# Optimization experiments

Hardware: AMD Instinct MI355X
Metric: run time of the kernel (lower is better)

## Reference

```python
import jax, jax.numpy as jnp
import numpy as np

H = 8          # num heads
LN_EPS = 1e-5  # torch LayerNorm default

_SHAPES = {
    'src': (1024, 8, 256), 'pos': (1024, 8, 256), 'query_embed': (80, 8, 256), 'cam_mask': (8, 80, 1024),
    'enc_qkv_w': (2, 768, 256), 'enc_qkv_b': (2, 768), 'enc_out_w': (2, 256, 256), 'enc_out_b': (2, 256),
    'enc_ln1_g': (2, 256), 'enc_ln1_b': (2, 256),
    'enc_ff1_w': (2, 2048, 256), 'enc_ff1_b': (2, 2048), 'enc_ff2_w': (2, 256, 2048), 'enc_ff2_b': (2, 256),
    'enc_ln2_g': (2, 256), 'enc_ln2_b': (2, 256),
    'dec_sa_qkv_w': (2, 768, 256), 'dec_sa_qkv_b': (2, 768), 'dec_sa_out_w': (2, 256, 256), 'dec_sa_out_b': (2, 256),
    'dec_ln1_g': (2, 256), 'dec_ln1_b': (2, 256),
    'dec_ca_qkv_w': (2, 768, 256), 'dec_ca_qkv_b': (2, 768), 'dec_ca_out_w': (2, 256, 256), 'dec_ca_out_b': (2, 256),
    'dec_ln2_g': (2, 256), 'dec_ln2_b': (2, 256),
    'dec_ff1_w': (2, 2048, 256), 'dec_ff1_b': (2, 2048), 'dec_ff2_w': (2, 256, 2048), 'dec_ff2_b': (2, 256),
    'dec_ln3_g': (2, 256), 'dec_ln3_b': (2, 256),
    'dec_norm_g': (256,), 'dec_norm_b': (256,),
}


def setup_inputs() -> dict:
    key = jax.random.key(0)
    out = {}
    for i, (name, sh) in enumerate(_SHAPES.items()):
        k = jax.random.fold_in(key, i)
        if name.endswith('_g'):
            out[name] = jnp.ones(sh, jnp.float32)
        elif name.endswith('ln1_b') or name.endswith('ln2_b') or name.endswith('ln3_b') or name == 'dec_norm_b':
            out[name] = jnp.zeros(sh, jnp.float32)
        else:
            scale = 1.0 if name in ('src', 'pos', 'query_embed', 'cam_mask') else 0.02
            out[name] = jax.random.normal(k, sh, dtype=jnp.float32) * scale
    return out


def layer_norm(x, g, b):
    mu = jnp.mean(x, axis=-1, keepdims=True)
    var = jnp.mean(jnp.square(x - mu), axis=-1, keepdims=True)
    return (x - mu) * jax.lax.rsqrt(var + LN_EPS) * g + b


def mha(q_in, k_in, v_in, qkv_w, qkv_b, out_w, out_b, bias=None):
    # q_in: [L,B,D], k_in/v_in: [S,B,D]; torch layout: projections are x @ W.T + b
    L, B, D = q_in.shape
    S = k_in.shape[0]
    hd = D // H
    wq, wk, wv = qkv_w[:D], qkv_w[D:2 * D], qkv_w[2 * D:]
    bq, bk, bv = qkv_b[:D], qkv_b[D:2 * D], qkv_b[2 * D:]
    q = (q_in @ wq.T + bq).reshape(L, B, H, hd).transpose(1, 2, 0, 3)  # [B,H,L,hd]
    k = (k_in @ wk.T + bk).reshape(S, B, H, hd).transpose(1, 2, 0, 3)  # [B,H,S,hd]
    v = (v_in @ wv.T + bv).reshape(S, B, H, hd).transpose(1, 2, 0, 3)
    logits = jnp.einsum('bhld,bhsd->bhls', q, k) * (1.0 / np.sqrt(hd))
    if bias is not None:
        logits = logits + bias[:, None, :, :]  # CAM bias broadcast over heads
    attn = jax.nn.softmax(logits, axis=-1)
    o = jnp.einsum('bhls,bhsd->bhld', attn, v).transpose(2, 0, 1, 3).reshape(L, B, D)
    return o @ out_w.T + out_b


def reference(src, pos, query_embed, cam_mask,
              enc_qkv_w, enc_qkv_b, enc_out_w, enc_out_b, enc_ln1_g, enc_ln1_b,
              enc_ff1_w, enc_ff1_b, enc_ff2_w, enc_ff2_b, enc_ln2_g, enc_ln2_b,
              dec_sa_qkv_w, dec_sa_qkv_b, dec_sa_out_w, dec_sa_out_b, dec_ln1_g, dec_ln1_b,
              dec_ca_qkv_w, dec_ca_qkv_b, dec_ca_out_w, dec_ca_out_b, dec_ln2_g, dec_ln2_b,
              dec_ff1_w, dec_ff1_b, dec_ff2_w, dec_ff2_b, dec_ln3_g, dec_ln3_b,
              dec_norm_g, dec_norm_b):
    n_enc = enc_qkv_w.shape[0]
    n_dec = dec_sa_qkv_w.shape[0]
    # --- encoder (post-norm DETR style, pos added to q,k) ---
    mem = src
    for i in range(n_enc):
        qk = mem + pos
        a = mha(qk, qk, mem, enc_qkv_w[i], enc_qkv_b[i], enc_out_w[i], enc_out_b[i])
        mem = layer_norm(mem + a, enc_ln1_g[i], enc_ln1_b[i])
        f = jax.nn.relu(mem @ enc_ff1_w[i].T + enc_ff1_b[i]) @ enc_ff2_w[i].T + enc_ff2_b[i]
        mem = layer_norm(mem + f, enc_ln2_g[i], enc_ln2_b[i])
    # --- decoder: tgt starts at zeros (Q2L), query_embed is query_pos ---
    tgt = jnp.zeros_like(query_embed)
    for i in range(n_dec):
        qk = tgt + query_embed
        sa = mha(qk, qk, tgt, dec_sa_qkv_w[i], dec_sa_qkv_b[i], dec_sa_out_w[i], dec_sa_out_b[i])
        tgt = layer_norm(tgt + sa, dec_ln1_g[i], dec_ln1_b[i])
        ca = mha(tgt + query_embed, mem + pos, mem,
                 dec_ca_qkv_w[i], dec_ca_qkv_b[i], dec_ca_out_w[i], dec_ca_out_b[i],
                 bias=cam_mask)  # MA: CAM-derived additive attention bias [B,L,S]
        tgt = layer_norm(tgt + ca, dec_ln2_g[i], dec_ln2_b[i])
        f = jax.nn.relu(tgt @ dec_ff1_w[i].T + dec_ff1_b[i]) @ dec_ff2_w[i].T + dec_ff2_b[i]
        tgt = layer_norm(tgt + f, dec_ln3_g[i], dec_ln3_b[i])
    out = layer_norm(tgt, dec_norm_g, dec_norm_b)
    return out[None]  # [1, L, B, D] as in TransformerDecoder's output.unsqueeze(0)
```

## Files before the change

### kernel.cpp

```cpp
#include <hip/hip_runtime.h>
#include <hip/hip_bf16.h>
#include <cstdint>
#include <cstddef>

typedef __hip_bfloat16 bf16;
typedef float f4 __attribute__((ext_vector_type(4)));
typedef float f32x4 __attribute__((ext_vector_type(4)));
typedef short s8v __attribute__((ext_vector_type(8)));
typedef unsigned short u16x4 __attribute__((ext_vector_type(4)));

#define LN_EPS 1e-5f
#define LOG2E 1.4426950408889634f

__device__ __forceinline__ void async_cp16(const void* g, void* lds) {
  __builtin_amdgcn_global_load_lds(
      (const __attribute__((address_space(1))) unsigned int*)g,
      (__attribute__((address_space(3))) unsigned int*)lds, 16, 0, 0);
}

__device__ __forceinline__ uint32_t pkbf(float lo, float hi) {
  bf16 a = __float2bfloat16(lo), c = __float2bfloat16(hi);
  return (uint32_t)*(unsigned short*)&a | ((uint32_t)*(unsigned short*)&c << 16);
}

#define NCAST 11
struct CastArgs {
  const float* in[NCAST];
  bf16* out[NCAST];
  int end4[NCAST];
  int nseg;
};

__global__ __launch_bounds__(256) void cast_multi(CastArgs a, int total4) {
  int i = blockIdx.x * 256 + threadIdx.x;
  if (i >= total4) return;
  int s = 0;
  while (i >= a.end4[s]) ++s;
  int j = i - (s ? a.end4[s - 1] : 0);
  f4 v = ((const f4*)a.in[s])[j];
  u16x4 o;
#pragma unroll
  for (int c = 0; c < 4; ++c) {
    bf16 h = __float2bfloat16(v[c]);
    o[c] = *reinterpret_cast<unsigned short*>(&h);
  }
  ((u16x4*)a.out[s])[j] = o;
}

__global__ __launch_bounds__(256) void scale_f32_kernel(const float* __restrict__ in,
                                                        float* __restrict__ out,
                                                        float s, int n4) {
  int i = blockIdx.x * 256 + threadIdx.x;
  if (i < n4) {
    f4 v = ((const f4*)in)[i];
    ((f4*)out)[i] = v * s;
  }
}

__global__ __launch_bounds__(256) void add_bf16_kernel(const float* __restrict__ a,
                                                       const float* __restrict__ b,
                                                       bf16* __restrict__ out, int n4) {
  int i = blockIdx.x * 256 + threadIdx.x;
  if (i < n4) {
    f4 x = ((const f4*)a)[i];
    f4 y = ((const f4*)b)[i];
    u16x4 o;
#pragma unroll
    for (int j = 0; j < 4; ++j) {
      bf16 h = __float2bfloat16(x[j] + y[j]);
      o[j] = *reinterpret_cast<unsigned short*>(&h);
    }
    ((u16x4*)out)[i] = o;
  }
}

template <int TB, int MODE, int SPLITK>
__global__ __launch_bounds__(256, 2) void mfma_gemm(
    const bf16* __restrict__ A, const bf16* __restrict__ W,
    const float* __restrict__ bias, float* __restrict__ C,
    bf16* __restrict__ Cb, int M, int N, int K, int HL, float qscale) {
  constexpr int WM = TB / 2, WN = TB / 2;
  constexpr int MR = WM / 16, NR = WN / 16;
  constexpr int NCH = TB / 32;
  __shared__ __attribute__((aligned(16))) unsigned short As[TB][64];
  __shared__ __attribute__((aligned(16))) unsigned short Ws[TB][64];
  const int tid = threadIdx.x;
  const int lane = tid & 63, wave = tid >> 6;
  const int wr = wave >> 1, wc = wave & 1;
  const int bm = blockIdx.x * TB, bn = blockIdx.y * TB;
  const int fr = lane & 15, fo = lane >> 4;
  const int srowi = lane >> 3;
  const int slot = lane & 7;
  const int gcol = (slot ^ srowi) * 8;

  const int kchunk = K / SPLITK;
  const int kbeg = (SPLITK > 1) ? blockIdx.z * kchunk : 0;

  f32x4 acc[MR][NR] = {};

  for (int k0 = kbeg; k0 < kbeg + kchunk; k0 += 64) {
    __syncthreads();
#pragma unroll
    for (int c = 0; c < NCH; ++c) {
      int rbase = wave * (TB / 4) + c * 8;
      int row = rbase + srowi;
      async_cp16(A + (size_t)(bm + row) * K + k0 + gcol, &As[rbase][0]);
      async_cp16(W + (size_t)(bn + row) * K + k0 + gcol, &Ws[rbase][0]);
    }
    __syncthreads();
#pragma unroll
    for (int ks = 0; ks < 2; ++ks) {
      s8v a[MR], b[NR];
#pragma unroll
      for (int mi = 0; mi < MR; ++mi) {
        int row = wr * WM + mi * 16 + fr;
        a[mi] = *(const s8v*)((const char*)&As[0][0] + row * 128 +
                              ((ks * 64 + fo * 16) ^ ((row & 7) << 4)));
      }
#pragma unroll
      for (int ni = 0; ni < NR; ++ni) {
        int row = wc * WN + ni * 16 + fr;
        b[ni] = *(const s8v*)((const char*)&Ws[0][0] + row * 128 +
                              ((ks * 64 + fo * 16) ^ ((row & 7) << 4)));
      }
#pragma unroll
      for (int mi = 0; mi < MR; ++mi)
#pragma unroll
        for (int ni = 0; ni < NR; ++ni)
          acc[mi][ni] = __builtin_amdgcn_mfma_f32_16x16x32_bf16(
              a[mi], b[ni], acc[mi][ni], 0, 0, 0);
    }
  }

  const int r0 = (lane >> 4) * 4;
  float* Cz = (MODE == 4) ? C + (size_t)blockIdx.z * M * N : C;
#pragma unroll
  for (int mi = 0; mi < MR; ++mi) {
#pragma unroll
    for (int ni = 0; ni < NR; ++ni) {
      int col = bn + wc * WN + ni * 16 + fr;
      float bv = (MODE == 4) ? 0.f : bias[col];
#pragma unroll
      for (int r = 0; r < 4; ++r) {
        int row = bm + wr * WM + mi * 16 + r0 + r;
        float t = acc[mi][ni][r] + bv;
        if (MODE == 2) t = fmaxf(t, 0.f);
        if (MODE == 0) {
          C[(size_t)row * N + col] = t;
        } else if (MODE == 4) {
          Cz[(size_t)row * N + col] = t;
        } else if (MODE == 3) {
          int l = row >> 3, bb = row & 7;
          int sec = col >> 8, hh = (col >> 5) & 7, d = col & 31;
          if (sec == 0) t *= qscale;
          Cb[(size_t)sec * ((size_t)64 * HL * 32) +
             ((size_t)(bb * 8 + hh) * HL + l) * 32 + d] = __float2bfloat16(t);
        } else if (MODE == 5) {
          int l = row >> 3, bb = row & 7;
          int hh = (col >> 5) & 7, d = col & 31;
          Cb[((size_t)(bb * 8 + hh) * 32 + d) * HL + l] = __float2bfloat16(t);
        } else {
          Cb[(size_t)row * N + col] = __float2bfloat16(t);
        }
      }
    }
  }
}

template <int HAS_BIAS, int PARTIAL>
__global__ __launch_bounds__(256, 4) void attn_mfma(
    const bf16* __restrict__ Qh, const bf16* __restrict__ Kh,
    const bf16* __restrict__ VhT, const float* __restrict__ bias,
    bf16* __restrict__ O, float* __restrict__ PO, float* __restrict__ PM,
    float* __restrict__ PL, int L, int S, int SC) {
  __shared__ __attribute__((aligned(16))) uint32_t Ps2[4][16][36];
  const int tid = threadIdx.x;
  const int lane = tid & 63, wave = tid >> 6;
  const int fr = lane & 15, fo = lane >> 4;
  const int bh = blockIdx.x;
  const int b = bh >> 3, h = bh & 7;
  const int q0 = blockIdx.y * 64 + wave * 16;
  const int q = q0 + fr;

  const int cz = PARTIAL ? blockIdx.z : 0;
  const int sb = PARTIAL ? cz * SC : 0;
  const int se = PARTIAL ? min(S, sb + SC) : S;

  s8v qf = {};
  if (q < L) qf = *(const s8v*)(Qh + ((size_t)bh * L + q) * 32 + fo * 8);

  const float* brow = nullptr;
  if (HAS_BIAS) brow = bias + ((size_t)b * L + (q < L ? q : L - 1)) * S;

  float m = -1e30f, lsum = 0.f;
  f32x4 oacc[2] = {};

  s8v kf[4];
#pragma unroll
  for (int kb = 0; kb < 4; ++kb)
    kf[kb] = *(const s8v*)(Kh + ((size_t)bh * S + sb + kb * 16 + fr) * 32 + fo * 8);

  for (int s0 = sb; s0 < se; s0 += 64) {
    const bool more = (s0 + 64 < se);
    s8v kn[4];
    if (more) {
#pragma unroll
      for (int kb = 0; kb < 4; ++kb)
        kn[kb] = *(const s8v*)(Kh + ((size_t)bh * S + s0 + 64 + kb * 16 + fr) * 32 + fo * 8);
    }
    s8v vf[2][2];
#pragma unroll
    for (int dh = 0; dh < 2; ++dh)
#pragma unroll
      for (int ks = 0; ks < 2; ++ks)
        vf[dh][ks] = *(const s8v*)(VhT + ((size_t)bh * 32 + dh * 16 + fr) * S +
                                   s0 + ks * 32 + fo * 8);
    f4 bias4[4];
    if (HAS_BIAS) {
#pragma unroll
      for (int kb = 0; kb < 4; ++kb)
        bias4[kb] = *(const f4*)(brow + s0 + kb * 16 + 4 * fo);
    }

    f32x4 sa[4];
#pragma unroll
    for (int kb = 0; kb < 4; ++kb) {
      f32x4 z = {};
      sa[kb] = __builtin_amdgcn_mfma_f32_16x16x32_bf16(kf[kb], qf, z, 0, 0, 0);
    }

    float lg[16];
#pragma unroll
    for (int kb = 0; kb < 4; ++kb)
#pragma unroll
      for (int r = 0; r < 4; ++r)
        lg[kb * 4 + r] = HAS_BIAS ? sa[kb][r] + bias4[kb][r] : sa[kb][r];

    if (s0 + 64 > se) {
#pragma unroll
      for (int kb = 0; kb < 4; ++kb)
#pragma unroll
        for (int r = 0; r < 4; ++r)
          if (s0 + kb * 16 + 4 * fo + r >= se) lg[kb * 4 + r] = -1e30f;
    }

    float tm = lg[0];
#pragma unroll
    for (int i = 1; i < 16; ++i) tm = fmaxf(tm, lg[i]);
    tm = fmaxf(tm, __shfl_xor(tm, 16));
    tm = fmaxf(tm, __shfl_xor(tm, 32));

    if (__any(tm > m + 8.f)) {
      float nm = fmaxf(m, tm);
      float rs = exp2f(m - nm);
      m = nm;
      lsum *= rs;
#pragma unroll
      for (int r = 0; r < 4; ++r) { oacc[0][r] *= rs; oacc[1][r] *= rs; }
    }

    float pr[16];
    float ps = 0.f;
#pragma unroll
    for (int i = 0; i < 16; ++i) {
      pr[i] = exp2f(lg[i] - m);
      ps += pr[i];
    }
    lsum += ps;

#pragma unroll
    for (int kb = 0; kb < 4; ++kb) {
      uint32_t w0 = pkbf(pr[kb * 4 + 0], pr[kb * 4 + 1]);
      uint32_t w1 = pkbf(pr[kb * 4 + 2], pr[kb * 4 + 3]);
      uint64_t w = (uint64_t)w0 | ((uint64_t)w1 << 32);
      *(uint64_t*)&Ps2[wave][fr][kb * 8 + 2 * fo] = w;
    }

    s8v pf[2];
#pragma unroll
    for (int ks = 0; ks < 2; ++ks)
      pf[ks] = *(const s8v*)&Ps2[wave][fr][ks * 16 + 4 * fo];

#pragma unroll
    for (int dh = 0; dh < 2; ++dh)
#pragma unroll
      for (int ks = 0; ks < 2; ++ks)
        oacc[dh] = __builtin_amdgcn_mfma_f32_16x16x32_bf16(
            vf[dh][ks], pf[ks], oacc[dh], 0, 0, 0);

    if (more) {
#pragma unroll
      for (int kb = 0; kb < 4; ++kb) kf[kb] = kn[kb];
    }
  }

  lsum += __shfl_xor(lsum, 16);
  lsum += __shfl_xor(lsum, 32);

  if (q < L) {
    if (PARTIAL) {
      size_t pi = ((size_t)cz * 64 + bh) * L + q;
      float* po = PO + pi * 32;
#pragma unroll
      for (int dh = 0; dh < 2; ++dh) {
        f4 t;
#pragma unroll
        for (int r = 0; r < 4; ++r) t[r] = oacc[dh][r];
        *(f4*)(po + dh * 16 + 4 * fo) = t;
      }
      if (fo == 0) { PM[pi] = m; PL[pi] = lsum; }
    } else {
      float inv = 1.f / lsum;
      bf16* op = O + ((size_t)q * 8 + b) * 256 + h * 32;
#pragma unroll
      for (int dh = 0; dh < 2; ++dh) {
        uint32_t w0 = pkbf(oacc[dh][0] * inv, oacc[dh][1] * inv);
        uint32_t w1 = pkbf(oacc[dh][2] * inv, oacc[dh][3] * inv);
        *(uint32_t*)(op + dh * 16 + 4 * fo) = w0;
        *(uint32_t*)(op + dh * 16 + 4 * fo + 2) = w1;
      }
    }
  }
}

__global__ __launch_bounds__(256) void attn_combine(
    const float* __restrict__ PO, const float* __restrict__ PM,
    const float* __restrict__ PL, bf16* __restrict__ O, int L, int NC) {
  int gid = blockIdx.x * 256 + threadIdx.x;
  if (gid >= 64 * L * 32) return;
  int d = gid & 31;
  int rem = gid >> 5;
  int q = rem % L, bh = rem / L;
  int b = bh >> 3, h = bh & 7;
  float M = -1e30f;
  for (int c = 0; c < NC; ++c) M = fmaxf(M, PM[((size_t)c * 64 + bh) * L + q]);
  float lsum = 0.f, o = 0.f;
  for (int c = 0; c < NC; ++c) {
    size_t pi = ((size_t)c * 64 + bh) * L + q;
    float w = exp2f(PM[pi] - M);
    lsum += PL[pi] * w;
    o += PO[pi * 32 + d] * w;
  }
  O[((size_t)q * 8 + b) * 256 + h * 32 + d] = __float2bfloat16(o / lsum);
}

__global__ __launch_bounds__(256) void ln_kernel(
    const float* __restrict__ x, const float* __restrict__ res,
    const float* __restrict__ parts, int nparts, int pstride,
    const float* __restrict__ gbias,
    const float* __restrict__ g, const float* __restrict__ b,
    float* __restrict__ out, bf16* __restrict__ outb) {
  const int row = blockIdx.x, tid = threadIdx.x;
  size_t idx = (size_t)row * 256 + tid;
  float v = x[idx];
  if (res) v += res[idx];
  if (parts) {
    for (int z = 0; z < nparts; ++z) v += parts[(size_t)z * pstride + idx];
  }
  if (gbias) v += gbias[tid];
  float s = v, s2 = v * v;
#pragma unroll
  for (int off = 32; off >= 1; off >>= 1) {
    s += __shfl_down(s, off);
    s2 += __shfl_down(s2, off);
  }
  __shared__ float red[8];
  int wv = tid >> 6;
  if ((tid & 63) == 0) { red[wv] = s; red[4 + wv] = s2; }
  __syncthreads();
  if (tid == 0) {
    float ts = red[0] + red[1] + red[2] + red[3];
    float ts2 = red[4] + red[5] + red[6] + red[7];
    float mu = ts * (1.f / 256.f);
    float var = ts2 * (1.f / 256.f) - mu * mu;
    red[0] = mu;
    red[1] = rsqrtf(var + LN_EPS);
  }
  __syncthreads();
  float y = (v - red[0]) * red[1] * g[tid] + b[tid];
  if (out) out[idx] = y;
  if (outb) outb[idx] = __float2bfloat16(y);
}

extern "C" void kernel_launch(void* const* d_in, const int* in_sizes, int n_in,
                              void* d_out, int out_size, void* d_ws, size_t ws_size,
                              hipStream_t stream) {
  const float* src         = (const float*)d_in[0];
  const float* pos         = (const float*)d_in[1];
  const float* query_embed = (const float*)d_in[2];
  const float* cam_mask    = (const float*)d_in[3];
  const float* enc_qkv_w   = (const float*)d_in[4];
  const float* enc_qkv_b   = (const float*)d_in[5];
  const float* enc_out_w   = (const float*)d_in[6];
  const float* enc_out_b   = (const float*)d_in[7];
  const float* enc_ln1_g   = (const float*)d_in[8];
  const float* enc_ln1_b   = (const float*)d_in[9];
  const float* enc_ff1_w   = (const float*)d_in[10];
  const float* enc_ff1_b   = (const float*)d_in[11];
  const float* enc_ff2_w   = (const float*)d_in[12];
  const float* enc_ff2_b   = (const float*)d_in[13];
  const float* enc_ln2_g   = (const float*)d_in[14];
  const float* enc_ln2_b   = (const float*)d_in[15];
  const float* dec_sa_qkv_w= (const float*)d_in[16];
  const float* dec_sa_qkv_b= (const float*)d_in[17];
  const float* dec_sa_out_w= (const float*)d_in[18];
  const float* dec_sa_out_b= (const float*)d_in[19];
  const float* dec_ln1_g   = (const float*)d_in[20];
  const float* dec_ln1_b   = (const float*)d_in[21];
  const float* dec_ca_qkv_w= (const float*)d_in[22];
  const float* dec_ca_qkv_b= (const float*)d_in[23];
  const float* dec_ca_out_w= (const float*)d_in[24];
  const float* dec_ca_out_b= (const float*)d_in[25];
  const float* dec_ln2_g   = (const float*)d_in[26];
  const float* dec_ln2_b   = (const float*)d_in[27];
  const float* dec_ff1_w   = (const float*)d_in[28];
  const float* dec_ff1_b   = (const float*)d_in[29];
  const float* dec_ff2_w   = (const float*)d_in[30];
  const float* dec_ff2_b   = (const float*)d_in[31];
  const float* dec_ln3_g   = (const float*)d_in[32];
  const float* dec_ln3_b   = (const float*)d_in[33];
  const float* dec_norm_g  = (const float*)d_in[34];
  const float* dec_norm_b  = (const float*)d_in[35];

  size_t off = 0;
  char* base = (char*)d_ws;
  auto af = [&](size_t n) { float* p = (float*)(base + off); off += n * 4; return p; };
  auto ab = [&](size_t n) { bf16*  p = (bf16*)(base + off);  off += n * 2; return p; };

  float* mem  = af(2097152);
  float* r1   = af(2097152);
  float* PO   = af(8388608);
  float* pm   = af(262144);
  float* pl   = af(262144);
  float* cmlog= af(655360);
  float* tgt  = af(163840);
  float* tpr  = af(163840);
  bf16* memb  = ab(2097152);
  bf16* qkb   = ab(2097152);
  bf16* aob   = ab(2097152);
  bf16* ffb   = ab(16777216);
  bf16* bufQ  = ab(4194304);
  bf16* bufK  = ab(2097152);
  bf16* bufV  = ab(2097152);
  bf16* tgtb  = ab(163840);
  bf16* tqkb  = ab(163840);
  bf16* taob  = ab(163840);
  bf16* tffb  = ab(1310720);
  bf16* w_enc_qkv = ab(393216);
  bf16* w_enc_out = ab(131072);
  bf16* w_enc_ff1 = ab(1048576);
  bf16* w_enc_ff2 = ab(1048576);
  bf16* w_sa_qkv  = ab(393216);
  bf16* w_sa_out  = ab(131072);
  bf16* w_ca_qkv  = ab(393216);
  bf16* w_ca_out  = ab(131072);
  bf16* w_dec_ff1 = ab(1048576);
  bf16* w_dec_ff2 = ab(1048576);

  const float qscale = 0.17677669529663687f * LOG2E;

  {
    CastArgs ca;
    const float* ins[NCAST] = {enc_qkv_w, enc_out_w, enc_ff1_w, enc_ff2_w,
                               dec_sa_qkv_w, dec_sa_out_w, dec_ca_qkv_w,
                               dec_ca_out_w, dec_ff1_w, dec_ff2_w, src};
    bf16* outs[NCAST] = {w_enc_qkv, w_enc_out, w_enc_ff1, w_enc_ff2,
                         w_sa_qkv, w_sa_out, w_ca_qkv,
                         w_ca_out, w_dec_ff1, w_dec_ff2, memb};
    int n4s[NCAST] = {98304, 32768, 262144, 262144, 98304, 32768, 98304,
                      32768, 262144, 262144, 524288};
    int acc = 0;
    for (int s = 0; s < NCAST; ++s) {
      ca.in[s] = ins[s]; ca.out[s] = outs[s];
      acc += n4s[s]; ca.end4[s] = acc;
    }
    ca.nseg = NCAST;
    cast_multi<<<(acc + 255) / 256, 256, 0, stream>>>(ca, acc);
  }
  scale_f32_kernel<<<640, 256, 0, stream>>>(cam_mask, cmlog, LOG2E, 163840);
  hipMemcpyAsync(mem, src, (size_t)2097152 * 4, hipMemcpyDeviceToDevice, stream);

  auto g64_f = [&](const bf16* A, const bf16* W, const float* bias, float* C,
                   int M, int N, int K) {
    mfma_gemm<64, 0, 1><<<dim3(M / 64, N / 64), 256, 0, stream>>>(
        A, W, bias, C, nullptr, M, N, K, 0, 1.f);
  };
  auto g64_head = [&](const bf16* A, const bf16* W, const float* bias, bf16* Cb,
                      int M, int N, int K, int HL, float qs) {
    mfma_gemm<64, 3, 1><<<dim3(M / 64, N / 64), 256, 0, stream>>>(
        A, W, bias, nullptr, Cb, M, N, K, HL, qs);
  };
  auto g64_headT = [&](const bf16* A, const bf16* W, const float* bias, bf16* Cb,
                       int M, int N, int K, int HL) {
    mfma_gemm<64, 5, 1><<<dim3(M / 64, N / 64), 256, 0, stream>>>(
        A, W, bias, nullptr, Cb, M, N, K, HL, 1.f);
  };
  auto g64_relu = [&](const bf16* A, const bf16* W, const float* bias, bf16* Cb,
                      int M, int N, int K) {
    mfma_gemm<64, 2, 1><<<dim3(M / 64, N / 64), 256, 0, stream>>>(
        A, W, bias, nullptr, Cb, M, N, K, 0, 1.f);
  };
  auto g128_relu = [&](const bf16* A, const bf16* W, const float* bias, bf16* Cb,
                       int M, int N, int K) {
    mfma_gemm<128, 2, 1><<<dim3(M / 128, N / 128), 256, 0, stream>>>(
        A, W, bias, nullptr, Cb, M, N, K, 0, 1.f);
  };

  for (int i = 0; i < 2; ++i) {
    const bf16* wq = w_enc_qkv + (size_t)i * 196608;
    const float* qkvb = enc_qkv_b + (size_t)i * 768;
    add_bf16_kernel<<<2048, 256, 0, stream>>>(mem, pos, qkb, 524288);
    g64_head(qkb, wq, qkvb, bufQ, 8192, 512, 256, 1024, qscale);
    g64_headT(memb, wq + 131072, qkvb + 512, bufV, 8192, 256, 256, 1024);
    attn_mfma<0, 0><<<dim3(64, 16), 256, 0, stream>>>(
        bufQ, bufQ + 2097152, bufV, nullptr, aob, nullptr, nullptr, nullptr,
        1024, 1024, 0);
    g64_f(aob, w_enc_out + (size_t)i * 65536, enc_out_b + i * 256, r1,
          8192, 256, 256);
    ln_kernel<<<8192, 256, 0, stream>>>(mem, r1, nullptr, 0, 0, nullptr,
                                        enc_ln1_g + i * 256, enc_ln1_b + i * 256,
                                        mem, memb);
    g128_relu(memb, w_enc_ff1 + (size_t)i * 524288, enc_ff1_b + i * 2048, ffb,
              8192, 2048, 256);
    mfma_gemm<128, 4, 4><<<dim3(64, 2, 4), 256, 0, stream>>>(
        ffb, w_enc_ff2 + (size_t)i * 524288, nullptr, PO, nullptr,
        8192, 256, 2048, 0, 1.f);
    ln_kernel<<<8192, 256, 0, stream>>>(mem, nullptr, PO, 4, 2097152,
                                        enc_ff2_b + i * 256,
                                        enc_ln2_g + i * 256, enc_ln2_b + i * 256,
                                        mem, memb);
  }

  hipMemsetAsync(tgt, 0, (size_t)163840 * 4, stream);
  hipMemsetAsync(tgtb, 0, (size_t)163840 * 2, stream);
  add_bf16_kernel<<<2048, 256, 0, stream>>>(mem, pos, qkb, 524288);

  for (int i = 0; i < 2; ++i) {
    const bf16* wsa = w_sa_qkv + (size_t)i * 196608;
    const float* sab = dec_sa_qkv_b + (size_t)i * 768;
    const bf16* wca = w_ca_qkv + (size_t)i * 196608;
    const float* cab = dec_ca_qkv_b + (size_t)i * 768;

    add_bf16_kernel<<<160, 256, 0, stream>>>(tgt, query_embed, tqkb, 40960);
    g64_head(tqkb, wsa, sab, bufQ, 640, 512, 256, 80, qscale);
    g64_headT(tgtb, wsa + 131072, sab + 512, bufV, 640, 256, 256, 80);
    attn_mfma<0, 0><<<dim3(64, 2), 256, 0, stream>>>(
        bufQ, bufQ + 163840, bufV, nullptr, taob, nullptr, nullptr, nullptr,
        80, 80, 0);
    g64_f(taob, w_sa_out + (size_t)i * 65536, dec_sa_out_b + i * 256, tpr,
          640, 256, 256);
    ln_kernel<<<640, 256, 0, stream>>>(tgt, tpr, nullptr, 0, 0, nullptr,
                                       dec_ln1_g + i * 256, dec_ln1_b + i * 256,
                                       tgt, tgtb);
    add_bf16_kernel<<<160, 256, 0, stream>>>(tgt, query_embed, tqkb, 40960);
    g64_head(tqkb, wca, cab, bufQ, 640, 256, 256, 80, qscale);
    g64_head(qkb, wca + 65536, cab + 256, bufK, 8192, 256, 256, 1024, 1.f);
    g64_headT(memb, wca + 131072, cab + 512, bufV, 8192, 256, 256, 1024);
    attn_mfma<1, 1><<<dim3(64, 2, 8), 256, 0, stream>>>(
        bufQ, bufK, bufV, cmlog, nullptr, PO, pm, pl, 80, 1024, 128);
    attn_combine<<<640, 256, 0, stream>>>(PO, pm, pl, taob, 80, 8);
    g64_f(taob, w_ca_out + (size_t)i * 65536, dec_ca_out_b + i * 256, tpr,
          640, 256, 256);
    ln_kernel<<<640, 256, 0, stream>>>(tgt, tpr, nullptr, 0, 0, nullptr,
                                       dec_ln2_g + i * 256, dec_ln2_b + i * 256,
                                       tgt, tgtb);
    g64_relu(tgtb, w_dec_ff1 + (size_t)i * 524288, dec_ff1_b + i * 2048, tffb,
             640, 2048, 256);
    mfma_gemm<64, 4, 4><<<dim3(10, 4, 4), 256, 0, stream>>>(
        tffb, w_dec_ff2 + (size_t)i * 524288, nullptr, PO, nullptr,
        640, 256, 2048, 0, 1.f);
    ln_kernel<<<640, 256, 0, stream>>>(tgt, nullptr, PO, 4, 163840,
                                       dec_ff2_b + i * 256,
                                       dec_ln3_g + i * 256, dec_ln3_b + i * 256,
                                       tgt, tgtb);
  }

  ln_kernel<<<640, 256, 0, stream>>>(tgt, nullptr, nullptr, 0, 0, nullptr,
                                     dec_norm_g, dec_norm_b,
                                     (float*)d_out, nullptr);
}
```

Measured before the change: 462.0 us.

## Batch decoder cross-attn K/V projections for both layers; split-K encoder attention

The memory-side K and V projections for cross-attention depend only on the final encoder memory, so both decoder layers' K/V weights are packed together and projected in one wide GEMM pair before the decoder loop. This replaces four smaller per-layer GEMMs with two larger ones. It needs reshuffled weight casts, a concatenated bias buffer and a section-aware transposed-V epilogue. Encoder self-attention is also switched to a two-way split over keys with a combine kernel, adding parallelism at the cost of extra partial-output traffic.

```diff
diff --git a/kernel.cpp b/kernel.cpp
--- a/kernel.cpp
+++ b/kernel.cpp
@@ -23,7 +23,7 @@
   return (uint32_t)*(unsigned short*)&a | ((uint32_t)*(unsigned short*)&c << 16);
 }
 
-#define NCAST 11
+#define NCAST 16
 struct CastArgs {
   const float* in[NCAST];
   bf16* out[NCAST];
@@ -157,8 +157,9 @@
              ((size_t)(bb * 8 + hh) * HL + l) * 32 + d] = __float2bfloat16(t);
         } else if (MODE == 5) {
           int l = row >> 3, bb = row & 7;
-          int hh = (col >> 5) & 7, d = col & 31;
-          Cb[((size_t)(bb * 8 + hh) * 32 + d) * HL + l] = __float2bfloat16(t);
+          int sec = col >> 8, hh = (col >> 5) & 7, d = col & 31;
+          Cb[(size_t)sec * ((size_t)64 * 32 * HL) +
+             ((size_t)(bb * 8 + hh) * 32 + d) * HL + l] = __float2bfloat16(t);
         } else {
           Cb[(size_t)row * N + col] = __float2bfloat16(t);
         }
@@ -433,6 +434,7 @@
   float* pm   = af(262144);
   float* pl   = af(262144);
   float* cmlog= af(655360);
+  float* pb   = af(1024);
   float* tgt  = af(163840);
   float* tpr  = af(163840);
   bf16* memb  = ab(2097152);
@@ -440,8 +442,9 @@
   bf16* aob   = ab(2097152);
   bf16* ffb   = ab(16777216);
   bf16* bufQ  = ab(4194304);
-  bf16* bufK  = ab(2097152);
-  bf16* bufV  = ab(2097152);
+  bf16* bufK  = ab(4194304);
+  bf16* bufV  = ab(4194304);
+  bf16* bufVsa= ab(163840);
   bf16* tgtb  = ab(163840);
   bf16* tqkb  = ab(163840);
   bf16* taob  = ab(163840);
@@ -452,7 +455,8 @@
   bf16* w_enc_ff2 = ab(1048576);
   bf16* w_sa_qkv  = ab(393216);
   bf16* w_sa_out  = ab(131072);
-  bf16* w_ca_qkv  = ab(393216);
+  bf16* w_ca_q    = ab(131072);
+  bf16* w_ca_kv   = ab(262144);
   bf16* w_ca_out  = ab(131072);
   bf16* w_dec_ff1 = ab(1048576);
   bf16* w_dec_ff2 = ab(1048576);
@@ -461,13 +465,28 @@
 
   {
     CastArgs ca;
-    const float* ins[NCAST] = {enc_qkv_w, enc_out_w, enc_ff1_w, enc_ff2_w,
-                               dec_sa_qkv_w, dec_sa_out_w, dec_ca_qkv_w,
-                               dec_ca_out_w, dec_ff1_w, dec_ff2_w, src};
-    bf16* outs[NCAST] = {w_enc_qkv, w_enc_out, w_enc_ff1, w_enc_ff2,
-                         w_sa_qkv, w_sa_out, w_ca_qkv,
-                         w_ca_out, w_dec_ff1, w_dec_ff2, memb};
-    int n4s[NCAST] = {98304, 32768, 262144, 262144, 98304, 32768, 98304,
+    const float* ins[NCAST] = {
+        enc_qkv_w, enc_out_w, enc_ff1_w, enc_ff2_w,
+        dec_sa_qkv_w, dec_sa_out_w,
+        dec_ca_qkv_w,
+        dec_ca_qkv_w + 65536,
+        dec_ca_qkv_w + 131072,
+        dec_ca_qkv_w + 196608,
+        dec_ca_qkv_w + 262144,
+        dec_ca_qkv_w + 327680,
+        dec_ca_out_w, dec_ff1_w, dec_ff2_w, src};
+    bf16* outs[NCAST] = {
+        w_enc_qkv, w_enc_out, w_enc_ff1, w_enc_ff2,
+        w_sa_qkv, w_sa_out,
+        w_ca_q,
+        w_ca_kv,
+        w_ca_kv + 131072,
+        w_ca_q + 65536,
+        w_ca_kv + 65536,
+        w_ca_kv + 196608,
+        w_ca_out, w_dec_ff1, w_dec_ff2, memb};
+    int n4s[NCAST] = {98304, 32768, 262144, 262144, 98304, 32768,
+                      16384, 16384, 16384, 16384, 16384, 16384,
                       32768, 262144, 262144, 524288};
     int acc = 0;
     for (int s = 0; s < NCAST; ++s) {
@@ -479,6 +498,10 @@
   }
   scale_f32_kernel<<<640, 256, 0, stream>>>(cam_mask, cmlog, LOG2E, 163840);
   hipMemcpyAsync(mem, src, (size_t)2097152 * 4, hipMemcpyDeviceToDevice, stream);
+  hipMemcpyAsync(pb,       dec_ca_qkv_b + 256,       1024, hipMemcpyDeviceToDevice, stream);
+  hipMemcpyAsync(pb + 256, dec_ca_qkv_b + 768 + 256, 1024, hipMemcpyDeviceToDevice, stream);
+  hipMemcpyAsync(pb + 512, dec_ca_qkv_b + 512,       1024, hipMemcpyDeviceToDevice, stream);
+  hipMemcpyAsync(pb + 768, dec_ca_qkv_b + 768 + 512, 1024, hipMemcpyDeviceToDevice, stream);
 
   auto g64_f = [&](const bf16* A, const bf16* W, const float* bias, float* C,
                    int M, int N, int K) {
@@ -512,9 +535,10 @@
     add_bf16_kernel<<<2048, 256, 0, stream>>>(mem, pos, qkb, 524288);
     g64_head(qkb, wq, qkvb, bufQ, 8192, 512, 256, 1024, qscale);
     g64_headT(memb, wq + 131072, qkvb + 512, bufV, 8192, 256, 256, 1024);
-    attn_mfma<0, 0><<<dim3(64, 16), 256, 0, stream>>>(
-        bufQ, bufQ + 2097152, bufV, nullptr, aob, nullptr, nullptr, nullptr,
-        1024, 1024, 0);
+    attn_mfma<0, 1><<<dim3(64, 16, 2), 256, 0, stream>>>(
+        bufQ, bufQ + 2097152, bufV, nullptr, nullptr, PO, pm, pl,
+        1024, 1024, 512);
+    attn_combine<<<8192, 256, 0, stream>>>(PO, pm, pl, aob, 1024, 2);
     g64_f(aob, w_enc_out + (size_t)i * 65536, enc_out_b + i * 256, r1,
           8192, 256, 256);
     ln_kernel<<<8192, 256, 0, stream>>>(mem, r1, nullptr, 0, 0, nullptr,
@@ -535,17 +559,19 @@
   hipMemsetAsync(tgtb, 0, (size_t)163840 * 2, stream);
   add_bf16_kernel<<<2048, 256, 0, stream>>>(mem, pos, qkb, 524288);
 
+  g64_head(qkb, w_ca_kv, pb, bufK, 8192, 512, 256, 1024, 1.f);
+  g64_headT(memb, w_ca_kv + 131072, pb + 512, bufV, 8192, 512, 256, 1024);
+
   for (int i = 0; i < 2; ++i) {
     const bf16* wsa = w_sa_qkv + (size_t)i * 196608;
     const float* sab = dec_sa_qkv_b + (size_t)i * 768;
-    const bf16* wca = w_ca_qkv + (size_t)i * 196608;
     const float* cab = dec_ca_qkv_b + (size_t)i * 768;
 
     add_bf16_kernel<<<160, 256, 0, stream>>>(tgt, query_embed, tqkb, 40960);
     g64_head(tqkb, wsa, sab, bufQ, 640, 512, 256, 80, qscale);
-    g64_headT(tgtb, wsa + 131072, sab + 512, bufV, 640, 256, 256, 80);
+    g64_headT(tgtb, wsa + 131072, sab + 512, bufVsa, 640, 256, 256, 80);
     attn_mfma<0, 0><<<dim3(64, 2), 256, 0, stream>>>(
-        bufQ, bufQ + 163840, bufV, nullptr, taob, nullptr, nullptr, nullptr,
+        bufQ, bufQ + 163840, bufVsa, nullptr, taob, nullptr, nullptr, nullptr,
         80, 80, 0);
     g64_f(taob, w_sa_out + (size_t)i * 65536, dec_sa_out_b + i * 256, tpr,
           640, 256, 256);
@@ -553,11 +579,10 @@
                                        dec_ln1_g + i * 256, dec_ln1_b + i * 256,
                                        tgt, tgtb);
     add_bf16_kernel<<<160, 256, 0, stream>>>(tgt, query_embed, tqkb, 40960);
-    g64_head(tqkb, wca, cab, bufQ, 640, 256, 256, 80, qscale);
-    g64_head(qkb, wca + 65536, cab + 256, bufK, 8192, 256, 256, 1024, 1.f);
-    g64_headT(memb, wca + 131072, cab + 512, bufV, 8192, 256, 256, 1024);
+    g64_head(tqkb, w_ca_q + (size_t)i * 65536, cab, bufQ, 640, 256, 256, 80, qscale);
     attn_mfma<1, 1><<<dim3(64, 2, 8), 256, 0, stream>>>(
-        bufQ, bufK, bufV, cmlog, nullptr, PO, pm, pl, 80, 1024, 128);
+        bufQ, bufK + (size_t)i * 2097152, bufV + (size_t)i * 2097152, cmlog,
+        nullptr, PO, pm, pl, 80, 1024, 128);
     attn_combine<<<640, 256, 0, stream>>>(PO, pm, pl, taob, 80, 8);
     g64_f(taob, w_ca_out + (size_t)i * 65536, dec_ca_out_b + i * 256, tpr,
           640, 256, 256);
```

Result: slower. 481.3 us (+4.2%).
